# Performance work log

Hardware: AMD Instinct MI355X
Metric: run time of the kernel (lower is better)

The kernel has to match this reference:

```python
import jax, jax.numpy as jnp
import numpy as np

INF = 1.0e12
B, S, HID, LAB = 8, 1024, 1024, 64
NAH = 16
HD = (HID + LAB) // NAH  # 68
SCALE = 1.0 / HD ** 0.5  # config.pointer_scale = True
P = 64  # padded num_positives per doc


def _rope_rotate(qw, kw):
    # SinusoidalPositionEmbedding(head_size, 'zero') + apply_rotary_position_embeddings
    s, hd = qw.shape[1], qw.shape[-1]
    pos = jnp.arange(s, dtype=jnp.float32)[:, None]
    inv = jnp.power(10000.0, -2.0 * jnp.arange(hd // 2, dtype=jnp.float32) / hd)
    ang = pos * inv  # [S, hd/2]; pos_emb interleaves (sin, cos)
    sin = jnp.repeat(jnp.sin(ang), 2, axis=-1)[None, :, None, :]  # [1,S,1,hd]
    cos = jnp.repeat(jnp.cos(ang), 2, axis=-1)[None, :, None, :]

    def rot(x):
        x2 = jnp.stack([-x[..., 1::2], x[..., ::2]], axis=-1).reshape(x.shape)
        return x * cos + x2 * sin

    return rot(qw), rot(kw)


def _global_pointer(x, W, b, mask, heads, rope, tril):
    bx, sx, _ = x.shape
    proj = (x @ W.T + b).reshape(bx, sx, heads, 2 * HD)
    qw, kw = proj[..., :HD], proj[..., HD:]
    if rope:
        qw, kw = _rope_rotate(qw, kw)
    logits = jnp.einsum('bmhd,bnhd->bhmn', qw, kw) * SCALE  # [B,H,S,S]
    pad = mask[:, None, None, :]  # masks key/column dim, as in torch code
    logits = logits * pad - (1.0 - pad) * INF
    if tril:
        logits = logits - jnp.tril(jnp.ones((sx, sx), logits.dtype), -1) * INF
    return logits


def _mcce(y_true, y_pred):
    # multilabel_categorical_crossentropy_v2 with mask_zero=True (gt padded with 0s)
    bx, hx, sx, _ = y_pred.shape
    flat = y_true[..., 0] * sx + y_true[..., 1]  # [B,H,P]
    yp = y_pred.reshape(bx, hx, sx * sx)
    zeros = jnp.zeros((bx, hx, 1), yp.dtype)
    yp = jnp.concatenate([yp, zeros], axis=-1)  # [B,H,S*S+1]
    infs = zeros + INF
    yp_pos = jnp.concatenate([infs, yp[..., 1:]], axis=-1)  # idx0 -> +INF
    bi = jnp.arange(bx)[:, None, None]
    hi = jnp.arange(hx)[None, :, None]
    y_pos2 = yp_pos[bi, hi, flat]
    y_pos1 = jnp.concatenate([y_pos2, zeros], axis=-1)
    yp_neg = jnp.concatenate([-infs, yp[..., 1:]], axis=-1)  # idx0 -> -INF
    y_pos2b = yp_neg[bi, hi, flat]
    yp_neg = yp_neg.at[bi, hi, flat].set(y_pos2b - INF)  # knock out positives
    yp_neg = jnp.concatenate([yp_neg, zeros], axis=-1)
    pos_loss = jax.nn.logsumexp(-y_pos1, axis=-1)
    neg_loss = jax.nn.logsumexp(yp_neg, axis=-1)
    return jnp.sum(pos_loss + neg_loss)


def setup_inputs():
    ks = jax.random.split(jax.random.key(0), 10)
    hidden = jax.random.normal(ks[0], (B, S, HID), jnp.float32)
    entity_labels = jax.random.randint(ks[1], (B, S), 0, 3, jnp.int32)
    attention_mask = jnp.ones((B, S), jnp.float32)
    gt_entity = jnp.sort(jax.random.randint(ks[2], (B, 2, P, 2), 0, S, jnp.int32), axis=-1)
    gt_head = jax.random.randint(ks[3], (B, 1, P, 2), 0, S, jnp.int32)
    gt_tail = jax.random.randint(ks[4], (B, 1, P, 2), 0, S, jnp.int32)
    d_in = HID + LAB  # 1088
    ent_emb = 0.02 * jax.random.normal(ks[5], (3, LAB), jnp.float32)
    W_ent = 0.03 * jax.random.normal(ks[6], (2 * 2 * HD, d_in), jnp.float32)
    b_ent = jnp.zeros((2 * 2 * HD,), jnp.float32)
    W_head = 0.03 * jax.random.normal(ks[7], (2 * HD, d_in), jnp.float32)
    b_head = jnp.zeros((2 * HD,), jnp.float32)
    W_tail = 0.03 * jax.random.normal(ks[8], (2 * HD, d_in), jnp.float32)
    b_tail = jnp.zeros((2 * HD,), jnp.float32)
    return dict(hidden=hidden, entity_labels=entity_labels, attention_mask=attention_mask,
                gt_entity=gt_entity, gt_head=gt_head, gt_tail=gt_tail, ent_emb=ent_emb,
                W_ent=W_ent, b_ent=b_ent, W_head=W_head, b_head=b_head,
                W_tail=W_tail, b_tail=b_tail)


def reference(hidden, entity_labels, attention_mask, gt_entity, gt_head, gt_tail,
              ent_emb, W_ent, b_ent, W_head, b_head, W_tail, b_tail):
    # label embedding concat (config.hidden_size += label_emb_size)
    x = jnp.concatenate([hidden, ent_emb[entity_labels]], axis=-1)  # [B,S,1088]
    ent_logits = _global_pointer(x, W_ent, b_ent, attention_mask, 2, True, True)
    head_logits = _global_pointer(x, W_head, b_head, attention_mask, 1, False, False)
    tail_logits = _global_pointer(x, W_tail, b_tail, attention_mask, 1, False, False)
    loss = _mcce(gt_entity, ent_logits) + _mcce(gt_head, head_logits) + _mcce(gt_tail, tail_logits)
    return loss
```

## Files before the change

### kernel.cpp

```cpp
#include <hip/hip_runtime.h>
#include <math.h>

#define B_    8
#define S_    1024
#define HID_  1024
#define DIN_  1088
#define HD_   68
#define P_    64
#define NJ    544
#define NJP   576
#define NTOK  8192

typedef short  bf16x8  __attribute__((ext_vector_type(8)));
typedef short  short4v __attribute__((ext_vector_type(4)));
typedef float  f32x4   __attribute__((ext_vector_type(4)));

static constexpr float SCALE_ = 0.121267812518166f;
static constexpr float CINV_  = -0.27089236388165246f;

__device__ __constant__ int qoffW[4] = {0, 136, 272, 408};
__device__ __constant__ int koffW[4] = {68, 204, 340, 476};

__device__ __forceinline__ short f2bf(float f) {
    unsigned u = __float_as_uint(f);
    unsigned r = (u + 0x7FFFu + ((u >> 16) & 1u)) >> 16;
    return (short)r;
}
__device__ __forceinline__ float b2f(short s) {
    return __uint_as_float(((unsigned)(unsigned short)s) << 16);
}

__global__ __launch_bounds__(256) void prep_kernel(
        const float* __restrict__ hidden, const float* __restrict__ ent_emb,
        const float* __restrict__ W_ent,  const float* __restrict__ b_ent,
        const float* __restrict__ W_head, const float* __restrict__ b_head,
        const float* __restrict__ W_tail, const float* __restrict__ b_tail,
        short* __restrict__ Hbf, short* __restrict__ Wbf,
        float* __restrict__ T, float* __restrict__ accbuf, float* __restrict__ outf) {
    const int bx = blockIdx.x, tid = threadIdx.x;
    if (bx < 4096) {
        const size_t i = ((size_t)bx * 256 + tid) * 8;
        float4 a = *(const float4*)(hidden + i);
        float4 b = *(const float4*)(hidden + i + 4);
        *(bf16x8*)(Hbf + i) = (bf16x8){f2bf(a.x), f2bf(a.y), f2bf(a.z), f2bf(a.w),
                                       f2bf(b.x), f2bf(b.y), f2bf(b.z), f2bf(b.w)};
    } else if (bx < 4096 + NJP) {
        const int j = bx - 4096;
        const float* wrow = nullptr;
        if (j < 272)      wrow = W_ent  + (size_t)j * DIN_;
        else if (j < 408) wrow = W_head + (size_t)(j - 272) * DIN_;
        else if (j < NJ)  wrow = W_tail + (size_t)(j - 408) * DIN_;
        short4v o;
        if (wrow) {
            float4 v = *(const float4*)(wrow + tid * 4);
            o = (short4v){f2bf(v.x), f2bf(v.y), f2bf(v.z), f2bf(v.w)};
        } else o = (short4v){0, 0, 0, 0};
        *(short4v*)&Wbf[(size_t)j * HID_ + tid * 4] = o;
    } else if (bx < 4096 + NJP + 9) {
        const int idx = bx - 4096 - NJP;
        const int l = idx / 3;
        const int j = (idx % 3) * 256 + tid;
        if (j >= NJ) return;
        const float* wrow; float bias;
        if (j < 272)      { wrow = W_ent  + (size_t)j * DIN_;         bias = b_ent[j];        }
        else if (j < 408) { wrow = W_head + (size_t)(j - 272) * DIN_; bias = b_head[j - 272]; }
        else              { wrow = W_tail + (size_t)(j - 408) * DIN_; bias = b_tail[j - 408]; }
        const float* e = ent_emb + l * 64;
        float s = bias;
        #pragma unroll 8
        for (int i = 0; i < 64; ++i) s += e[i] * wrow[HID_ + i];
        T[l * NJ + j] = s;
    } else {
        if (tid == 0) *outf = 0.f;
        for (int i = tid; i < 512; i += 256) accbuf[i] = 0.f;
    }
}

__global__ __launch_bounds__(256) void proj_kernel(
        const short* __restrict__ Hbf, const int* __restrict__ labels,
        const short* __restrict__ Wbf, const float* __restrict__ T,
        short* __restrict__ Cbuf) {
    __shared__ __align__(16) short As[128 * 72];
    __shared__ __align__(16) short Bs[64 * 72];
    const int m0 = blockIdx.y * 128;
    const int n0 = blockIdx.x * 64;
    const int tid = threadIdx.x;
    const int lane = tid & 63, wave = tid >> 6;
    const int wm = wave * 32;
    const int lrow = lane & 15, lk = (lane >> 4) * 8;

    f32x4 acc[2][4] = {};

    for (int kk = 0; kk < HID_; kk += 64) {
        __syncthreads();
        #pragma unroll
        for (int i = 0; i < 4; ++i) {
            const int c = i * 256 + tid;
            const int row = c >> 3, ch = (c & 7) * 8;
            *(bf16x8*)&As[row * 72 + ch] =
                *(const bf16x8*)(Hbf + (size_t)(m0 + row) * HID_ + kk + ch);
        }
        #pragma unroll
        for (int i = 0; i < 2; ++i) {
            const int c = i * 256 + tid;
            const int row = c >> 3, ch = (c & 7) * 8;
            *(bf16x8*)&Bs[row * 72 + ch] =
                *(const bf16x8*)(Wbf + (size_t)(n0 + row) * HID_ + kk + ch);
        }
        __syncthreads();
        #pragma unroll
        for (int ks = 0; ks < 2; ++ks) {
            const int k = ks * 32 + lk;
            bf16x8 a0 = *(const bf16x8*)&As[(wm + 0  + lrow) * 72 + k];
            bf16x8 a1 = *(const bf16x8*)&As[(wm + 16 + lrow) * 72 + k];
            #pragma unroll
            for (int nj = 0; nj < 4; ++nj) {
                bf16x8 bb = *(const bf16x8*)&Bs[(nj * 16 + lrow) * 72 + k];
                acc[0][nj] = __builtin_amdgcn_mfma_f32_16x16x32_bf16(a0, bb, acc[0][nj], 0, 0, 0);
                acc[1][nj] = __builtin_amdgcn_mfma_f32_16x16x32_bf16(a1, bb, acc[1][nj], 0, 0, 0);
            }
        }
    }

    __syncthreads();
    #pragma unroll
    for (int mi = 0; mi < 2; ++mi) {
        #pragma unroll
        for (int r = 0; r < 4; ++r) {
            const int rl = wm + mi * 16 + (lane >> 4) * 4 + r;
            const int gm = m0 + rl;
            const int lab = labels[gm];
            const float* Trow = T + lab * NJ;
            const int s = gm & (S_ - 1);
            #pragma unroll
            for (int nj = 0; nj < 4; ++nj) {
                const int cl = nj * 16 + lrow;
                const int gj = n0 + cl;
                float v = acc[mi][nj][r] + ((gj < NJ) ? Trow[gj] : 0.f);
                float vp = __shfl_xor(v, 1);
                float res = v;
                if (gj < 272) {
                    const int matb = (gj >= 136) ? 136 : 0;
                    const int within = gj - matb;
                    const int d = (within < HD_) ? within : within - HD_;
                    float inv = __expf((float)(d >> 1) * CINV_);
                    float ang = (float)s * inv;
                    float sn, cs;
                    __sincosf(ang, &sn, &cs);
                    res = (lane & 1) ? (v * cs + vp * sn) : (v * cs - vp * sn);
                }
                As[rl * 72 + cl] = f2bf(res);
            }
        }
    }
    __syncthreads();
    #pragma unroll
    for (int i = 0; i < 4; ++i) {
        const int c = i * 256 + tid;
        const int row = c >> 3, piece = c & 7;
        uint4 vv = *(const uint4*)&As[row * 72 + piece * 8];
        *(uint4*)&Cbuf[(size_t)(m0 + row) * NJP + n0 + piece * 8] = vv;
    }
}

__global__ __launch_bounds__(256, 4) void negsum_kernel(const short* __restrict__ Cbuf,
                                                        float* __restrict__ accbuf) {
    const int id = blockIdx.x;
    const int xcd = id & 7, slot = id >> 3;
    const int bz = xcd * 4 + (slot >> 5);
    const int sub = slot & 31;
    const int grp = sub >> 1, kh = sub & 1;
    const int mat = bz >> 3, b = bz & 7;
    const bool ent = mat < 2;
    const int tid = threadIdx.x, lane = tid & 63, wave = tid >> 6;
    const int lrow = lane & 15, lkg = lane >> 4;
    const int m0w = (grp * 4 + wave) * 16;
    const int t0 = ent ? (m0w >> 6) : 0;
    const int tstart = (8 * kh > t0) ? 8 * kh : t0;
    const int tend = 8 * kh + 8;

    float sum = 0.f;
    if (tstart < tend) {
        const unsigned keep = (lkg == 0) ? 0xFFFFFFFFu : 0u;
        const size_t rowQ = (size_t)(b * S_ + m0w + lrow) * NJP + qoffW[mat] + lkg * 8;
        bf16x8 q0 = *(const bf16x8*)(Cbuf + rowQ);
        bf16x8 q1 = *(const bf16x8*)(Cbuf + rowQ + 32);
        bf16x8 q2 = *(const bf16x8*)(Cbuf + rowQ + 64);
        { uint4* u = (uint4*)&q2; u->x &= keep; u->y &= keep; u->z = 0u; u->w = 0u; }

        const size_t kbase = (size_t)(b * S_) * NJP + koffW[mat] + lkg * 8;
        for (int t = tstart; t < tend; ++t) {
            f32x4 acc[4] = {};
            #pragma unroll
            for (int nj = 0; nj < 4; ++nj) {
                const size_t rowK = kbase + (size_t)(t * 64 + nj * 16 + lrow) * NJP;
                bf16x8 k0 = *(const bf16x8*)(Cbuf + rowK);
                bf16x8 k1 = *(const bf16x8*)(Cbuf + rowK + 32);
                bf16x8 k2 = *(const bf16x8*)(Cbuf + rowK + 64);
                { uint4* u = (uint4*)&k2; u->x &= keep; u->y &= keep; u->z = 0u; u->w = 0u; }
                acc[nj] = __builtin_amdgcn_mfma_f32_16x16x32_bf16(q0, k0, acc[nj], 0, 0, 0);
                acc[nj] = __builtin_amdgcn_mfma_f32_16x16x32_bf16(q1, k1, acc[nj], 0, 0, 0);
                acc[nj] = __builtin_amdgcn_mfma_f32_16x16x32_bf16(q2, k2, acc[nj], 0, 0, 0);
            }
            const bool needmask = (ent && t == t0) || (t == 0 && m0w == 0);
            if (needmask) {
                #pragma unroll
                for (int nj = 0; nj < 4; ++nj)
                    #pragma unroll
                    for (int r = 0; r < 4; ++r) {
                        const int gm = m0w + lkg * 4 + r;
                        const int gn = t * 64 + nj * 16 + lrow;
                        const bool valid = (!ent || gm <= gn) && ((gm | gn) != 0);
                        sum += valid ? __expf(acc[nj][r] * SCALE_) : 0.f;
                    }
            } else {
                #pragma unroll
                for (int nj = 0; nj < 4; ++nj)
                    #pragma unroll
                    for (int r = 0; r < 4; ++r)
                        sum += __expf(acc[nj][r] * SCALE_);
            }
        }
        #pragma unroll
        for (int off = 32; off; off >>= 1) sum += __shfl_down(sum, off);
        if (lane == 0) atomicAdd(&accbuf[bz * 16 + grp], sum);
    }
}

__global__ void final_kernel(const short* __restrict__ Cbuf,
                             const int* __restrict__ gt_ent, const int* __restrict__ gt_head,
                             const int* __restrict__ gt_tail,
                             const float* __restrict__ accbuf, float* __restrict__ out) {
    const int bz = blockIdx.x;
    const int mat = bz >> 3, b = bz & 7;
    const int p = threadIdx.x;
    int r, c;
    if (mat < 2)       { const int* g = gt_ent  + (((b * 2 + mat) * P_) + p) * 2; r = g[0]; c = g[1]; }
    else if (mat == 2) { const int* g = gt_head + (b * P_ + p) * 2;               r = g[0]; c = g[1]; }
    else               { const int* g = gt_tail + (b * P_ + p) * 2;               r = g[0]; c = g[1]; }
    const int flat = r * S_ + c;

    const short* q = Cbuf + (size_t)(b * S_ + r) * NJP + qoffW[mat];
    const short* k = Cbuf + (size_t)(b * S_ + c) * NJP + koffW[mat];
    float dot = 0.f;
    #pragma unroll 4
    for (int d = 0; d < HD_; ++d) dot += b2f(q[d]) * b2f(k[d]);
    const float logit = dot * SCALE_;

    float pos = (flat != 0) ? __expf(-logit) : 0.f;

    __shared__ int flats[P_];
    flats[p] = flat;
    __syncthreads();
    bool first = true;
    for (int pp = 0; pp < p; ++pp) if (flats[pp] == flat) first = false;
    float excl = (flat != 0 && first) ? __expf(logit) : 0.f;

    #pragma unroll
    for (int off = 32; off; off >>= 1) {
        pos  += __shfl_down(pos,  off);
        excl += __shfl_down(excl, off);
    }
    if (p == 0) {
        float neg = 0.f;
        #pragma unroll
        for (int i = 0; i < 16; ++i) neg += accbuf[bz * 16 + i];
        float loss = logf(1.f + pos) + logf(2.f + neg - excl);
        atomicAdd(out, loss);
    }
}

extern "C" void kernel_launch(void* const* d_in, const int* in_sizes, int n_in,
                              void* d_out, int out_size, void* d_ws, size_t ws_size,
                              hipStream_t stream) {
    const float* hidden  = (const float*)d_in[0];
    const int*   labels  = (const int*)  d_in[1];
    const int*   gt_ent  = (const int*)  d_in[3];
    const int*   gt_head = (const int*)  d_in[4];
    const int*   gt_tail = (const int*)  d_in[5];
    const float* ent_emb = (const float*)d_in[6];
    const float* W_ent   = (const float*)d_in[7];
    const float* b_ent   = (const float*)d_in[8];
    const float* W_head  = (const float*)d_in[9];
    const float* b_head  = (const float*)d_in[10];
    const float* W_tail  = (const float*)d_in[11];
    const float* b_tail  = (const float*)d_in[12];

    char* base = (char*)d_ws;
    float* T      = (float*)base;
    float* accbuf = (float*)(base + 8192);
    short* Wbf  = (short*)(base + 16384);
    short* Hbf  = (short*)(base + 2 * 1024 * 1024);
    short* Cbuf = (short*)(base + 19 * 1024 * 1024);
    float* outf = (float*)d_out;

    prep_kernel<<<4096 + NJP + 9 + 1, 256, 0, stream>>>(
        hidden, ent_emb, W_ent, b_ent, W_head, b_head, W_tail, b_tail,
        Hbf, Wbf, T, accbuf, outf);
    proj_kernel<<<dim3(NJP / 64, NTOK / 128), 256, 0, stream>>>(Hbf, labels, Wbf, T, Cbuf);
    negsum_kernel<<<1024, 256, 0, stream>>>(Cbuf, accbuf);
    final_kernel<<<32, 64, 0, stream>>>(Cbuf, gt_ent, gt_head, gt_tail, accbuf, outf);
}
```

Baseline: 185.3 us.

## Pad projection heads to 96-wide slices and stage K tiles in shared memory

Each 68-wide q/k head slice now gets its own zero-padded 96-column slot, so per-head data is aligned and the masking of the third k-chunk goes away. The negsum kernel now loads each 64-row K tile cooperatively into double-buffered LDS with register prefetch of the next tile, and all four waves share it instead of each reading K straight from global memory. The cost is a wider projection GEMM (768 vs 576 columns, more padded MFMA work and a larger Cbuf), plus two barriers per tile.

```diff
diff --git a/kernel.cpp b/kernel.cpp
--- a/kernel.cpp
+++ b/kernel.cpp
@@ -7,9 +7,11 @@
 #define DIN_  1088
 #define HD_   68
 #define P_    64
-#define NJ    544
-#define NJP   576
+#define NSL   8
+#define SLW   96
+#define NJP   768
 #define NTOK  8192
+#define LSTR  104
 
 typedef short  bf16x8  __attribute__((ext_vector_type(8)));
 typedef short  short4v __attribute__((ext_vector_type(4)));
@@ -17,9 +19,6 @@
 
 static constexpr float SCALE_ = 0.121267812518166f;
 static constexpr float CINV_  = -0.27089236388165246f;
-
-__device__ __constant__ int qoffW[4] = {0, 136, 272, 408};
-__device__ __constant__ int koffW[4] = {68, 204, 340, 476};
 
 __device__ __forceinline__ short f2bf(float f) {
     unsigned u = __float_as_uint(f);
@@ -46,10 +45,14 @@
                                        f2bf(b.x), f2bf(b.y), f2bf(b.z), f2bf(b.w)};
     } else if (bx < 4096 + NJP) {
         const int j = bx - 4096;
+        const int slice = j / SLW, w = j - slice * SLW;
         const float* wrow = nullptr;
-        if (j < 272)      wrow = W_ent  + (size_t)j * DIN_;
-        else if (j < 408) wrow = W_head + (size_t)(j - 272) * DIN_;
-        else if (j < NJ)  wrow = W_tail + (size_t)(j - 408) * DIN_;
+        if (w < HD_) {
+            const int actual = slice * HD_ + w;
+            if (actual < 272)      wrow = W_ent  + (size_t)actual * DIN_;
+            else if (actual < 408) wrow = W_head + (size_t)(actual - 272) * DIN_;
+            else                   wrow = W_tail + (size_t)(actual - 408) * DIN_;
+        }
         short4v o;
         if (wrow) {
             float4 v = *(const float4*)(wrow + tid * 4);
@@ -60,16 +63,20 @@
         const int idx = bx - 4096 - NJP;
         const int l = idx / 3;
         const int j = (idx % 3) * 256 + tid;
-        if (j >= NJ) return;
-        const float* wrow; float bias;
-        if (j < 272)      { wrow = W_ent  + (size_t)j * DIN_;         bias = b_ent[j];        }
-        else if (j < 408) { wrow = W_head + (size_t)(j - 272) * DIN_; bias = b_head[j - 272]; }
-        else              { wrow = W_tail + (size_t)(j - 408) * DIN_; bias = b_tail[j - 408]; }
-        const float* e = ent_emb + l * 64;
-        float s = bias;
-        #pragma unroll 8
-        for (int i = 0; i < 64; ++i) s += e[i] * wrow[HID_ + i];
-        T[l * NJ + j] = s;
+        const int slice = j / SLW, w = j - slice * SLW;
+        float s = 0.f;
+        if (w < HD_) {
+            const int actual = slice * HD_ + w;
+            const float* wrow; float bias;
+            if (actual < 272)      { wrow = W_ent  + (size_t)actual * DIN_;         bias = b_ent[actual];        }
+            else if (actual < 408) { wrow = W_head + (size_t)(actual - 272) * DIN_; bias = b_head[actual - 272]; }
+            else                   { wrow = W_tail + (size_t)(actual - 408) * DIN_; bias = b_tail[actual - 408]; }
+            const float* e = ent_emb + l * 64;
+            s = bias;
+            #pragma unroll 8
+            for (int i = 0; i < 64; ++i) s += e[i] * wrow[HID_ + i];
+        }
+        T[l * NJP + j] = s;
     } else {
         if (tid == 0) *outf = 0.f;
         for (int i = tid; i < 512; i += 256) accbuf[i] = 0.f;
@@ -130,19 +137,17 @@
             const int rl = wm + mi * 16 + (lane >> 4) * 4 + r;
             const int gm = m0 + rl;
             const int lab = labels[gm];
-            const float* Trow = T + lab * NJ;
+            const float* Trow = T + lab * NJP;
             const int s = gm & (S_ - 1);
             #pragma unroll
             for (int nj = 0; nj < 4; ++nj) {
                 const int cl = nj * 16 + lrow;
                 const int gj = n0 + cl;
-                float v = acc[mi][nj][r] + ((gj < NJ) ? Trow[gj] : 0.f);
+                float v = acc[mi][nj][r] + Trow[gj];
                 float vp = __shfl_xor(v, 1);
                 float res = v;
-                if (gj < 272) {
-                    const int matb = (gj >= 136) ? 136 : 0;
-                    const int within = gj - matb;
-                    const int d = (within < HD_) ? within : within - HD_;
+                if (gj < 384) {
+                    const int d = gj % SLW;
                     float inv = __expf((float)(d >> 1) * CINV_);
                     float ang = (float)s * inv;
                     float sn, cs;
@@ -169,62 +174,93 @@
     const int xcd = id & 7, slot = id >> 3;
     const int bz = xcd * 4 + (slot >> 5);
     const int sub = slot & 31;
-    const int grp = sub >> 1, kh = sub & 1;
+    const int mc = sub >> 1, kh = sub & 1;
     const int mat = bz >> 3, b = bz & 7;
     const bool ent = mat < 2;
-    const int tid = threadIdx.x, lane = tid & 63, wave = tid >> 6;
-    const int lrow = lane & 15, lkg = lane >> 4;
-    const int m0w = (grp * 4 + wave) * 16;
-    const int t0 = ent ? (m0w >> 6) : 0;
-    const int tstart = (8 * kh > t0) ? 8 * kh : t0;
+    const int tstart = ent ? ((8 * kh > mc) ? 8 * kh : mc) : 8 * kh;
     const int tend = 8 * kh + 8;
+    if (tstart >= tend) return;
+
+    __shared__ __align__(16) short Ks[2][64 * LSTR];
+    const int tid = threadIdx.x;
+    const int lane = tid & 63, wave = tid >> 6;
+    const int lrow = lane & 15, lk8 = (lane >> 4) * 8;
+    const int m0w = mc * 64 + wave * 16;
+
+    bf16x8 qa[3];
+    {
+        const size_t rowQ = (size_t)(b * S_ + m0w + lrow) * NJP + mat * 192 + lk8;
+        #pragma unroll
+        for (int ks = 0; ks < 3; ++ks)
+            qa[ks] = *(const bf16x8*)(Cbuf + rowQ + ks * 32);
+    }
+
+    const size_t kslice = (size_t)(b * S_) * NJP + mat * 192 + 96;
+    uint4 kreg[3];
+    {
+        const size_t kb = kslice + (size_t)tstart * 64 * NJP;
+        #pragma unroll
+        for (int i = 0; i < 3; ++i) {
+            const int c = i * 256 + tid;
+            const int row = c / 12, u = c - row * 12;
+            kreg[i] = *(const uint4*)(Cbuf + kb + (size_t)row * NJP + u * 8);
+        }
+    }
 
     float sum = 0.f;
-    if (tstart < tend) {
-        const unsigned keep = (lkg == 0) ? 0xFFFFFFFFu : 0u;
-        const size_t rowQ = (size_t)(b * S_ + m0w + lrow) * NJP + qoffW[mat] + lkg * 8;
-        bf16x8 q0 = *(const bf16x8*)(Cbuf + rowQ);
-        bf16x8 q1 = *(const bf16x8*)(Cbuf + rowQ + 32);
-        bf16x8 q2 = *(const bf16x8*)(Cbuf + rowQ + 64);
-        { uint4* u = (uint4*)&q2; u->x &= keep; u->y &= keep; u->z = 0u; u->w = 0u; }
-
-        const size_t kbase = (size_t)(b * S_) * NJP + koffW[mat] + lkg * 8;
-        for (int t = tstart; t < tend; ++t) {
-            f32x4 acc[4] = {};
+    for (int t = tstart; t < tend; ++t) {
+        const int buf = (t - tstart) & 1;
+        #pragma unroll
+        for (int i = 0; i < 3; ++i) {
+            const int c = i * 256 + tid;
+            const int row = c / 12, u = c - row * 12;
+            *(uint4*)&Ks[buf][row * LSTR + u * 8] = kreg[i];
+        }
+        __syncthreads();
+        if (t + 1 < tend) {
+            const size_t kb = kslice + (size_t)(t + 1) * 64 * NJP;
+            #pragma unroll
+            for (int i = 0; i < 3; ++i) {
+                const int c = i * 256 + tid;
+                const int row = c / 12, u = c - row * 12;
+                kreg[i] = *(const uint4*)(Cbuf + kb + (size_t)row * NJP + u * 8);
+            }
+        }
+
+        f32x4 acc[4] = {};
+        #pragma unroll
+        for (int ks = 0; ks < 3; ++ks) {
             #pragma unroll
             for (int nj = 0; nj < 4; ++nj) {
-                const size_t rowK = kbase + (size_t)(t * 64 + nj * 16 + lrow) * NJP;
-                bf16x8 k0 = *(const bf16x8*)(Cbuf + rowK);
-                bf16x8 k1 = *(const bf16x8*)(Cbuf + rowK + 32);
-                bf16x8 k2 = *(const bf16x8*)(Cbuf + rowK + 64);
-                { uint4* u = (uint4*)&k2; u->x &= keep; u->y &= keep; u->z = 0u; u->w = 0u; }
-                acc[nj] = __builtin_amdgcn_mfma_f32_16x16x32_bf16(q0, k0, acc[nj], 0, 0, 0);
-                acc[nj] = __builtin_amdgcn_mfma_f32_16x16x32_bf16(q1, k1, acc[nj], 0, 0, 0);
-                acc[nj] = __builtin_amdgcn_mfma_f32_16x16x32_bf16(q2, k2, acc[nj], 0, 0, 0);
+                bf16x8 kb8 = *(const bf16x8*)&Ks[buf][(nj * 16 + lrow) * LSTR + ks * 32 + lk8];
+                acc[nj] = __builtin_amdgcn_mfma_f32_16x16x32_bf16(qa[ks], kb8, acc[nj], 0, 0, 0);
             }
-            const bool needmask = (ent && t == t0) || (t == 0 && m0w == 0);
-            if (needmask) {
+        }
+
+        const bool needmask = (ent && t == mc) || (t == 0 && m0w == 0);
+        if (needmask) {
+            #pragma unroll
+            for (int nj = 0; nj < 4; ++nj)
                 #pragma unroll
-                for (int nj = 0; nj < 4; ++nj)
-                    #pragma unroll
-                    for (int r = 0; r < 4; ++r) {
-                        const int gm = m0w + lkg * 4 + r;
-                        const int gn = t * 64 + nj * 16 + lrow;
-                        const bool valid = (!ent || gm <= gn) && ((gm | gn) != 0);
-                        sum += valid ? __expf(acc[nj][r] * SCALE_) : 0.f;
-                    }
-            } else {
+                for (int r = 0; r < 4; ++r) {
+                    const int gm = m0w + (lane >> 4) * 4 + r;
+                    const int gn = t * 64 + nj * 16 + lrow;
+                    const bool valid = (!ent || gm <= gn) && ((gm | gn) != 0);
+                    sum += valid ? __expf(acc[nj][r] * SCALE_) : 0.f;
+                }
+        } else {
+            #pragma unroll
+            for (int nj = 0; nj < 4; ++nj)
                 #pragma unroll
-                for (int nj = 0; nj < 4; ++nj)
-                    #pragma unroll
-                    for (int r = 0; r < 4; ++r)
-                        sum += __expf(acc[nj][r] * SCALE_);
-            }
-        }
-        #pragma unroll
-        for (int off = 32; off; off >>= 1) sum += __shfl_down(sum, off);
-        if (lane == 0) atomicAdd(&accbuf[bz * 16 + grp], sum);
-    }
+                for (int r = 0; r < 4; ++r)
+                    sum += __expf(acc[nj][r] * SCALE_);
+        }
+        __syncthreads();
+    }
+
+    #pragma unroll
+    for (int off = 32; off; off >>= 1) sum += __shfl_down(sum, off);
+    if (lane == 0) atomicAdd(&accbuf[bz * 16 + mc], sum);
 }
 
 __global__ void final_kernel(const short* __restrict__ Cbuf,
@@ -240,8 +276,8 @@
     else               { const int* g = gt_tail + (b * P_ + p) * 2;               r = g[0]; c = g[1]; }
     const int flat = r * S_ + c;
 
-    const short* q = Cbuf + (size_t)(b * S_ + r) * NJP + qoffW[mat];
-    const short* k = Cbuf + (size_t)(b * S_ + c) * NJP + koffW[mat];
+    const short* q = Cbuf + (size_t)(b * S_ + r) * NJP + mat * 192;
+    const short* k = Cbuf + (size_t)(b * S_ + c) * NJP + mat * 192 + 96;
     float dot = 0.f;
     #pragma unroll 4
     for (int d = 0; d < HD_; ++d) dot += b2f(q[d]) * b2f(k[d]);
@@ -288,7 +324,7 @@
 
     char* base = (char*)d_ws;
     float* T      = (float*)base;
-    float* accbuf = (float*)(base + 8192);
+    float* accbuf = (float*)(base + 12288);
     short* Wbf  = (short*)(base + 16384);
     short* Hbf  = (short*)(base + 2 * 1024 * 1024);
     short* Cbuf = (short*)(base + 19 * 1024 * 1024);
```

Result: faster. 170.1 us (-8.2%).
